# Kernel tuning notes

Hardware: AMD Instinct MI355X
Metric: run time of the kernel (lower is better)

## Reference

```python
import jax, jax.numpy as jnp
import numpy as np

OUT_F, IN_F = 4096, 4096
BLOCK = 64  # bitsandbytes NF4 block size

# NF4 code table (bitsandbytes): 16 quantile levels of a standard normal, scaled to [-1, 1]
NF4_CODE = jnp.array([
    -1.0, -0.6961928009986877, -0.5250730514526367, -0.39491748809814453,
    -0.28444138169288635, -0.18477343022823334, -0.09105003625154495, 0.0,
    0.07958029955625534, 0.16093020141124725, 0.24611230194568634, 0.33791524171829224,
    0.44070982933044434, 0.5626170039176941, 0.7229568362236023, 1.0,
], dtype=jnp.float32)


def dequantize_nf4(packed, absmax):
    # packed: [OUT_F*IN_F//2] int values in [0,256); two 4-bit indices per byte (high nibble first)
    hi = (packed >> 4) & 0xF
    lo = packed & 0xF
    idx = jnp.stack([hi, lo], axis=-1).reshape(-1)           # [OUT_F*IN_F]
    vals = NF4_CODE[idx]                                      # lookup
    vals = vals.reshape(-1, BLOCK) * absmax[:, None]          # per-block scale
    return vals.reshape(OUT_F, IN_F)


def setup_inputs() -> dict:
    key = jax.random.key(0)
    k1, k2, k3, k4 = jax.random.split(key, 4)
    x = jax.random.normal(k1, (4, 2048, IN_F), dtype=jnp.float32)
    packed_weight = jax.random.randint(k2, (OUT_F * IN_F // 2,), 0, 256, dtype=jnp.int32)
    absmax = jax.random.uniform(k3, (OUT_F * IN_F // BLOCK,), dtype=jnp.float32)
    bias = jax.random.normal(k4, (OUT_F,), dtype=jnp.float32)
    return {"x": x, "packed_weight": packed_weight, "absmax": absmax, "bias": bias}


def reference(x, packed_weight, absmax, bias):
    weight = dequantize_nf4(packed_weight, absmax)            # [OUT_F, IN_F]
    # F.linear: x @ W^T + b
    return jnp.einsum('bsi,oi->bso', x, weight) + bias
```

## Files before the change

kernel.cpp:

```cpp
#include <hip/hip_runtime.h>
#include <hip/hip_bf16.h>
#include <stdint.h>

#define IN_F   4096
#define OUT_F  4096
#define MROWS  8192

typedef __bf16 bf16x8 __attribute__((ext_vector_type(8)));
typedef float  f32x4  __attribute__((ext_vector_type(4)));
typedef unsigned short ushort8v __attribute__((ext_vector_type(8)));

__device__ __constant__ float NF4_TAB[16] = {
    -1.0f, -0.6961928009986877f, -0.5250730514526367f, -0.39491748809814453f,
    -0.28444138169288635f, -0.18477343022823334f, -0.09105003625154495f, 0.0f,
    0.07958029955625534f, 0.16093020141124725f, 0.24611230194568634f, 0.33791524171829224f,
    0.44070982933044434f, 0.5626170039176941f, 0.7229568362236023f, 1.0f,
};

__device__ __forceinline__ unsigned short f2bf_rne(float f) {
    unsigned u = __builtin_bit_cast(unsigned, f);
    return (unsigned short)((u + 0x7FFFu + ((u >> 16) & 1u)) >> 16);
}

__global__ void dequant_nf4_kernel(const int* __restrict__ packed,
                                   const float* __restrict__ absmax,
                                   unsigned short* __restrict__ wout,
                                   int ngroups) {
    int stride = gridDim.x * blockDim.x;
    for (int g = blockIdx.x * blockDim.x + threadIdx.x; g < ngroups; g += stride) {
        int4 pv = reinterpret_cast<const int4*>(packed)[g];
        float am = absmax[g >> 3];
        int p0 = pv.x, p1 = pv.y, p2 = pv.z, p3 = pv.w;
        ushort8v o;
        o[0] = f2bf_rne(NF4_TAB[(p0 >> 4) & 0xF] * am);
        o[1] = f2bf_rne(NF4_TAB[ p0       & 0xF] * am);
        o[2] = f2bf_rne(NF4_TAB[(p1 >> 4) & 0xF] * am);
        o[3] = f2bf_rne(NF4_TAB[ p1       & 0xF] * am);
        o[4] = f2bf_rne(NF4_TAB[(p2 >> 4) & 0xF] * am);
        o[5] = f2bf_rne(NF4_TAB[ p2       & 0xF] * am);
        o[6] = f2bf_rne(NF4_TAB[(p3 >> 4) & 0xF] * am);
        o[7] = f2bf_rne(NF4_TAB[ p3       & 0xF] * am);
        *reinterpret_cast<ushort8v*>(&wout[(size_t)g * 8]) = o;
    }
}

__global__ void cvt_f32_bf16_kernel(const float* __restrict__ in,
                                    unsigned short* __restrict__ out,
                                    int ngroups) {
    int stride = gridDim.x * blockDim.x;
    for (int g = blockIdx.x * blockDim.x + threadIdx.x; g < ngroups; g += stride) {
        float4 v = reinterpret_cast<const float4*>(in)[g];
        ushort4 o;
        o.x = f2bf_rne(v.x);
        o.y = f2bf_rne(v.y);
        o.z = f2bf_rne(v.z);
        o.w = f2bf_rne(v.w);
        reinterpret_cast<ushort4*>(out)[g] = o;
    }
}

#define GLOAD16(gp, lp)                                                        \
    __builtin_amdgcn_global_load_lds(                                          \
        (const __attribute__((address_space(1))) void*)(gp),                   \
        (__attribute__((address_space(3))) void*)(lp), 16, 0, 0)

__global__ __launch_bounds__(256) void gemm_bf16_kernel(
        const unsigned short* __restrict__ A,
        const unsigned short* __restrict__ B,
        const float* __restrict__ bias,
        float* __restrict__ C) {
    __shared__ __align__(16) unsigned short As[128 * 32];
    __shared__ __align__(16) unsigned short Bs[128 * 32];

    const int tid  = threadIdx.x;
    const int lane = tid & 63;
    const int wave = tid >> 6;
    const int wr = wave >> 1;
    const int wc = wave & 1;
    const int lr = lane & 15;
    const int lg = lane >> 4;

    const int bn = (blockIdx.x & 31) << 7;
    const int bm = (blockIdx.x >> 5) << 7;

    f32x4 acc[4][4] = {};

    const int c1 = tid, c2 = tid + 256;
    const int r1 = c1 >> 2, k1 = (c1 & 3) * 8;
    const int r2 = c2 >> 2, k2 = (c2 & 3) * 8;
    const unsigned short* Ag1 = A + (size_t)(bm + r1) * IN_F + k1;
    const unsigned short* Ag2 = A + (size_t)(bm + r2) * IN_F + k2;
    const unsigned short* Bg1 = B + (size_t)(bn + r1) * IN_F + k1;
    const unsigned short* Bg2 = B + (size_t)(bn + r2) * IN_F + k2;

    for (int k0 = 0; k0 < IN_F; k0 += 32) {
        GLOAD16(Ag1 + k0, &As[c1 * 8]);
        GLOAD16(Ag2 + k0, &As[c2 * 8]);
        GLOAD16(Bg1 + k0, &Bs[c1 * 8]);
        GLOAD16(Bg2 + k0, &Bs[c2 * 8]);
        __syncthreads();

        bf16x8 af[4], bfv[4];
#pragma unroll
        for (int mi = 0; mi < 4; ++mi)
            af[mi] = *reinterpret_cast<const bf16x8*>(
                &As[(wr * 64 + mi * 16 + lr) * 32 + lg * 8]);
#pragma unroll
        for (int ni = 0; ni < 4; ++ni)
            bfv[ni] = *reinterpret_cast<const bf16x8*>(
                &Bs[(wc * 64 + ni * 16 + lr) * 32 + lg * 8]);

#pragma unroll
        for (int mi = 0; mi < 4; ++mi)
#pragma unroll
            for (int ni = 0; ni < 4; ++ni)
                acc[mi][ni] = __builtin_amdgcn_mfma_f32_16x16x32_bf16(
                    af[mi], bfv[ni], acc[mi][ni], 0, 0, 0);

        __syncthreads();
    }

#pragma unroll
    for (int mi = 0; mi < 4; ++mi) {
        const int row0 = bm + wr * 64 + mi * 16 + lg * 4;
#pragma unroll
        for (int ni = 0; ni < 4; ++ni) {
            const int col = bn + wc * 64 + ni * 16 + lr;
            const float bs = bias[col];
            float* cp = C + (size_t)row0 * OUT_F + col;
#pragma unroll
            for (int j = 0; j < 4; ++j)
                cp[(size_t)j * OUT_F] = acc[mi][ni][j] + bs;
        }
    }
}

extern "C" void kernel_launch(void* const* d_in, const int* in_sizes, int n_in,
                              void* d_out, int out_size, void* d_ws, size_t ws_size,
                              hipStream_t stream) {
    const float* x      = (const float*)d_in[0];
    const int*   packed = (const int*)d_in[1];
    const float* absmax = (const float*)d_in[2];
    const float* bias   = (const float*)d_in[3];
    float* out = (float*)d_out;

    unsigned short* Wb = (unsigned short*)d_ws;
    unsigned short* Xb = Wb + (size_t)OUT_F * IN_F;

    const int npacked_groups = (OUT_F * IN_F / 2) / 4;
    const int ncvt_groups    = (MROWS * IN_F) / 4;

    dequant_nf4_kernel<<<2048, 256, 0, stream>>>(packed, absmax, Wb, npacked_groups);
    cvt_f32_bf16_kernel<<<2048, 256, 0, stream>>>(x, Xb, ncvt_groups);
    gemm_bf16_kernel<<<dim3(2048), dim3(256), 0, stream>>>(Xb, Wb, bias, out);
}
```

Baseline: 556.5 us.

## Merge prep kernels and replace GEMM with 256x256 double-buffered swizzled kernel

Combines weight dequantization and activation bf16 conversion into one launch that splits blocks between the two jobs, with the NF4 table copied into shared memory. The GEMM moves from 128x128 tiles with a single LDS buffer to 256x256 tiles on 512 threads, using a double-buffered 128KB LDS pipeline, XOR-swizzled layout, staged prefetch with explicit vmcnt/lgkmcnt waits, setprio around MFMA bursts, and a remapped block order for L2 locality. The aim is more data reuse per tile and overlap of global loads with MFMA work. In exchange it uses many more registers and all LDS, so occupancy drops to one block per CU, and the hand-written wait counts are fragile.

```diff
diff --git a/kernel.cpp b/kernel.cpp
--- a/kernel.cpp
+++ b/kernel.cpp
@@ -5,6 +5,7 @@
 #define IN_F   4096
 #define OUT_F  4096
 #define MROWS  8192
+#define NT     64
 
 typedef __bf16 bf16x8 __attribute__((ext_vector_type(8)));
 typedef float  f32x4  __attribute__((ext_vector_type(4)));
@@ -22,40 +23,45 @@
     return (unsigned short)((u + 0x7FFFu + ((u >> 16) & 1u)) >> 16);
 }
 
-__global__ void dequant_nf4_kernel(const int* __restrict__ packed,
-                                   const float* __restrict__ absmax,
-                                   unsigned short* __restrict__ wout,
-                                   int ngroups) {
-    int stride = gridDim.x * blockDim.x;
-    for (int g = blockIdx.x * blockDim.x + threadIdx.x; g < ngroups; g += stride) {
-        int4 pv = reinterpret_cast<const int4*>(packed)[g];
-        float am = absmax[g >> 3];
-        int p0 = pv.x, p1 = pv.y, p2 = pv.z, p3 = pv.w;
-        ushort8v o;
-        o[0] = f2bf_rne(NF4_TAB[(p0 >> 4) & 0xF] * am);
-        o[1] = f2bf_rne(NF4_TAB[ p0       & 0xF] * am);
-        o[2] = f2bf_rne(NF4_TAB[(p1 >> 4) & 0xF] * am);
-        o[3] = f2bf_rne(NF4_TAB[ p1       & 0xF] * am);
-        o[4] = f2bf_rne(NF4_TAB[(p2 >> 4) & 0xF] * am);
-        o[5] = f2bf_rne(NF4_TAB[ p2       & 0xF] * am);
-        o[6] = f2bf_rne(NF4_TAB[(p3 >> 4) & 0xF] * am);
-        o[7] = f2bf_rne(NF4_TAB[ p3       & 0xF] * am);
-        *reinterpret_cast<ushort8v*>(&wout[(size_t)g * 8]) = o;
-    }
-}
-
-__global__ void cvt_f32_bf16_kernel(const float* __restrict__ in,
-                                    unsigned short* __restrict__ out,
-                                    int ngroups) {
-    int stride = gridDim.x * blockDim.x;
-    for (int g = blockIdx.x * blockDim.x + threadIdx.x; g < ngroups; g += stride) {
-        float4 v = reinterpret_cast<const float4*>(in)[g];
-        ushort4 o;
-        o.x = f2bf_rne(v.x);
-        o.y = f2bf_rne(v.y);
-        o.z = f2bf_rne(v.z);
-        o.w = f2bf_rne(v.w);
-        reinterpret_cast<ushort4*>(out)[g] = o;
+__global__ __launch_bounds__(256) void prep_kernel(
+        const float* __restrict__ x, const int* __restrict__ packed,
+        const float* __restrict__ absmax,
+        unsigned short* __restrict__ Wb, unsigned short* __restrict__ Xb) {
+    __shared__ float tab[16];
+    if (threadIdx.x < 16) tab[threadIdx.x] = NF4_TAB[threadIdx.x];
+    __syncthreads();
+
+    const int bid = blockIdx.x;
+    if (bid < 512) {
+        const int ngroups = OUT_F * IN_F / 8;
+        const int stride = 512 * 256;
+        for (int g = bid * 256 + threadIdx.x; g < ngroups; g += stride) {
+            int4 pv = reinterpret_cast<const int4*>(packed)[g];
+            float am = absmax[g >> 3];
+            ushort8v o;
+            o[0] = f2bf_rne(tab[(pv.x >> 4) & 0xF] * am);
+            o[1] = f2bf_rne(tab[ pv.x       & 0xF] * am);
+            o[2] = f2bf_rne(tab[(pv.y >> 4) & 0xF] * am);
+            o[3] = f2bf_rne(tab[ pv.y       & 0xF] * am);
+            o[4] = f2bf_rne(tab[(pv.z >> 4) & 0xF] * am);
+            o[5] = f2bf_rne(tab[ pv.z       & 0xF] * am);
+            o[6] = f2bf_rne(tab[(pv.w >> 4) & 0xF] * am);
+            o[7] = f2bf_rne(tab[ pv.w       & 0xF] * am);
+            *reinterpret_cast<ushort8v*>(&Wb[(size_t)g * 8]) = o;
+        }
+    } else {
+        const int ngroups = MROWS * IN_F / 8;
+        const int stride = 1536 * 256;
+        for (int g = (bid - 512) * 256 + threadIdx.x; g < ngroups; g += stride) {
+            float4 v0 = reinterpret_cast<const float4*>(x)[2 * g];
+            float4 v1 = reinterpret_cast<const float4*>(x)[2 * g + 1];
+            ushort8v o;
+            o[0] = f2bf_rne(v0.x); o[1] = f2bf_rne(v0.y);
+            o[2] = f2bf_rne(v0.z); o[3] = f2bf_rne(v0.w);
+            o[4] = f2bf_rne(v1.x); o[5] = f2bf_rne(v1.y);
+            o[6] = f2bf_rne(v1.z); o[7] = f2bf_rne(v1.w);
+            *reinterpret_cast<ushort8v*>(&Xb[(size_t)g * 8]) = o;
+        }
     }
 }
 
@@ -64,73 +70,130 @@
         (const __attribute__((address_space(1))) void*)(gp),                   \
         (__attribute__((address_space(3))) void*)(lp), 16, 0, 0)
 
-__global__ __launch_bounds__(256) void gemm_bf16_kernel(
+#define BAR()   __builtin_amdgcn_s_barrier()
+#define LGKM0() do { asm volatile("s_waitcnt lgkmcnt(0)" ::: "memory");        \
+                     __builtin_amdgcn_sched_barrier(0); } while (0)
+#define VMW(n)  asm volatile("s_waitcnt vmcnt(" #n ")" ::: "memory")
+
+__global__ __launch_bounds__(512) void gemm256_kernel(
         const unsigned short* __restrict__ A,
         const unsigned short* __restrict__ B,
         const float* __restrict__ bias,
         float* __restrict__ C) {
-    __shared__ __align__(16) unsigned short As[128 * 32];
-    __shared__ __align__(16) unsigned short Bs[128 * 32];
+    __shared__ __align__(16) unsigned short lds[65536];
 
     const int tid  = threadIdx.x;
     const int lane = tid & 63;
     const int wave = tid >> 6;
-    const int wr = wave >> 1;
-    const int wc = wave & 1;
-    const int lr = lane & 15;
-    const int lg = lane >> 4;
-
-    const int bn = (blockIdx.x & 31) << 7;
-    const int bm = (blockIdx.x >> 5) << 7;
-
-    f32x4 acc[4][4] = {};
-
-    const int c1 = tid, c2 = tid + 256;
-    const int r1 = c1 >> 2, k1 = (c1 & 3) * 8;
-    const int r2 = c2 >> 2, k2 = (c2 & 3) * 8;
-    const unsigned short* Ag1 = A + (size_t)(bm + r1) * IN_F + k1;
-    const unsigned short* Ag2 = A + (size_t)(bm + r2) * IN_F + k2;
-    const unsigned short* Bg1 = B + (size_t)(bn + r1) * IN_F + k1;
-    const unsigned short* Bg2 = B + (size_t)(bn + r2) * IN_F + k2;
-
-    for (int k0 = 0; k0 < IN_F; k0 += 32) {
-        GLOAD16(Ag1 + k0, &As[c1 * 8]);
-        GLOAD16(Ag2 + k0, &As[c2 * 8]);
-        GLOAD16(Bg1 + k0, &Bs[c1 * 8]);
-        GLOAD16(Bg2 + k0, &Bs[c2 * 8]);
-        __syncthreads();
-
-        bf16x8 af[4], bfv[4];
-#pragma unroll
-        for (int mi = 0; mi < 4; ++mi)
-            af[mi] = *reinterpret_cast<const bf16x8*>(
-                &As[(wr * 64 + mi * 16 + lr) * 32 + lg * 8]);
-#pragma unroll
-        for (int ni = 0; ni < 4; ++ni)
-            bfv[ni] = *reinterpret_cast<const bf16x8*>(
-                &Bs[(wc * 64 + ni * 16 + lr) * 32 + lg * 8]);
-
-#pragma unroll
-        for (int mi = 0; mi < 4; ++mi)
-#pragma unroll
-            for (int ni = 0; ni < 4; ++ni)
-                acc[mi][ni] = __builtin_amdgcn_mfma_f32_16x16x32_bf16(
-                    af[mi], bfv[ni], acc[mi][ni], 0, 0, 0);
-
-        __syncthreads();
-    }
-
-#pragma unroll
-    for (int mi = 0; mi < 4; ++mi) {
-        const int row0 = bm + wr * 64 + mi * 16 + lg * 4;
+    const int wr   = wave >> 2;
+    const int wcn  = wave & 3;
+    const int lr   = lane & 15;
+    const int lg   = lane >> 4;
+
+    const int bid = blockIdx.x;
+    const int wg  = (bid & 7) * 64 + (bid >> 3);
+    const int bm  = (wg >> 4) << 8;
+    const int bn  = (wg & 15) << 8;
+
+    int srow[2], skel[2];
+#pragma unroll
+    for (int r = 0; r < 2; ++r) {
+        int c = tid + r * 512;
+        int L = c * 16;
+        int sw = L ^ (((L >> 7) & 7) << 4);
+        srow[r] = sw >> 6;
+        skel[r] = (sw & 63) >> 1;
+    }
+    const unsigned short* pA0 = A + (size_t)(bm + srow[0]) * IN_F + skel[0];
+    const unsigned short* pA1 = A + (size_t)(bm + srow[1]) * IN_F + skel[1];
+    const unsigned short* pB0 = B + (size_t)(bn + srow[0]) * IN_F + skel[0];
+    const unsigned short* pB1 = B + (size_t)(bn + srow[1]) * IN_F + skel[1];
+    const int d0 = tid * 8, d1 = tid * 8 + 4096;
+
+#define STAGE_A(t, kh) do {                                                    \
+        int _b = ((t) & 1) * 32768 + (kh) * 8192;                              \
+        int _k = (t) * 64 + (kh) * 32;                                         \
+        GLOAD16(pA0 + _k, &lds[_b + d0]);                                      \
+        GLOAD16(pA1 + _k, &lds[_b + d1]); } while (0)
+#define STAGE_B(t, kh) do {                                                    \
+        int _b = ((t) & 1) * 32768 + 16384 + (kh) * 8192;                      \
+        int _k = (t) * 64 + (kh) * 32;                                         \
+        GLOAD16(pB0 + _k, &lds[_b + d0]);                                      \
+        GLOAD16(pB1 + _k, &lds[_b + d1]); } while (0)
+
+    const int laneoff = ((lr * 64 + lg * 16) ^ (((lr >> 1) & 7) << 4)) >> 1;
+    const int arow = wr * 128;
+    const int brow = wcn * 64;
+
+    f32x4  acc[8][4] = {};
+    bf16x8 af[4], bfv[4];
+
+#define LOADB(b, kh) do {                                                      \
+        int _base = (b) * 32768 + 16384 + (kh) * 8192 + brow * 32 + laneoff;   \
+        bfv[0] = *reinterpret_cast<const bf16x8*>(&lds[_base]);                \
+        bfv[1] = *reinterpret_cast<const bf16x8*>(&lds[_base + 512]);          \
+        bfv[2] = *reinterpret_cast<const bf16x8*>(&lds[_base + 1024]);         \
+        bfv[3] = *reinterpret_cast<const bf16x8*>(&lds[_base + 1536]); } while (0)
+#define LOADA(b, kh, mq) do {                                                  \
+        int _base = (b) * 32768 + (kh) * 8192 + (arow + (mq) * 64) * 32 + laneoff; \
+        af[0] = *reinterpret_cast<const bf16x8*>(&lds[_base]);                 \
+        af[1] = *reinterpret_cast<const bf16x8*>(&lds[_base + 512]);           \
+        af[2] = *reinterpret_cast<const bf16x8*>(&lds[_base + 1024]);          \
+        af[3] = *reinterpret_cast<const bf16x8*>(&lds[_base + 1536]); } while (0)
+
+#define MFMA16(mq) do {                                                        \
+        __builtin_amdgcn_s_setprio(1);                                         \
+        _Pragma("unroll")                                                      \
+        for (int mi = 0; mi < 4; ++mi)                                         \
+            _Pragma("unroll")                                                  \
+            for (int ni = 0; ni < 4; ++ni)                                     \
+                acc[(mq) * 4 + mi][ni] = __builtin_amdgcn_mfma_f32_16x16x32_bf16( \
+                    af[mi], bfv[ni], acc[(mq) * 4 + mi][ni], 0, 0, 0);         \
+        __builtin_amdgcn_s_setprio(0); } while (0)
+
+    STAGE_B(0, 0); STAGE_A(0, 0); STAGE_B(0, 1); STAGE_A(0, 1);
+    STAGE_B(1, 0); STAGE_A(1, 0); STAGE_B(1, 1);
+    VMW(6);
+    BAR();
+
+#pragma unroll 2
+    for (int t = 0; t < NT; ++t) {
+        const int b = t & 1;
+        LOADB(b, 0); LOADA(b, 0, 0);
+        if (t + 1 < NT) STAGE_A(t + 1, 1);
+        BAR(); LGKM0();
+        MFMA16(0);
+        BAR();
+        LOADA(b, 0, 1);
+        if (t + 2 < NT) STAGE_B(t + 2, 0);
+        BAR(); LGKM0();
+        MFMA16(1);
+        BAR();
+        LOADB(b, 1); LOADA(b, 1, 0);
+        if (t + 2 < NT) STAGE_A(t + 2, 0);
+        BAR(); LGKM0();
+        MFMA16(0);
+        BAR();
+        LOADA(b, 1, 1);
+        if (t + 2 < NT) STAGE_B(t + 2, 1);
+        BAR(); LGKM0();
+        MFMA16(1);
+        if (t < NT - 2)       { VMW(6); }
+        else if (t == NT - 2) { VMW(0); }
+        BAR();
+    }
+
+#pragma unroll
+    for (int a = 0; a < 8; ++a) {
+        const int row0 = bm + wr * 128 + (a >> 2) * 64 + (a & 3) * 16 + lg * 4;
 #pragma unroll
         for (int ni = 0; ni < 4; ++ni) {
-            const int col = bn + wc * 64 + ni * 16 + lr;
+            const int col = bn + wcn * 64 + ni * 16 + lr;
             const float bs = bias[col];
             float* cp = C + (size_t)row0 * OUT_F + col;
 #pragma unroll
             for (int j = 0; j < 4; ++j)
-                cp[(size_t)j * OUT_F] = acc[mi][ni][j] + bs;
+                cp[(size_t)j * OUT_F] = acc[a][ni][j] + bs;
         }
     }
 }
@@ -147,10 +210,6 @@
     unsigned short* Wb = (unsigned short*)d_ws;
     unsigned short* Xb = Wb + (size_t)OUT_F * IN_F;
 
-    const int npacked_groups = (OUT_F * IN_F / 2) / 4;
-    const int ncvt_groups    = (MROWS * IN_F) / 4;
-
-    dequant_nf4_kernel<<<2048, 256, 0, stream>>>(packed, absmax, Wb, npacked_groups);
-    cvt_f32_bf16_kernel<<<2048, 256, 0, stream>>>(x, Xb, ncvt_groups);
-    gemm_bf16_kernel<<<dim3(2048), dim3(256), 0, stream>>>(Xb, Wb, bias, out);
-}
+    prep_kernel<<<2048, 256, 0, stream>>>(x, packed, absmax, Wb, Xb);
+    gemm256_kernel<<<512, 512, 0, stream>>>(Xb, Wb, bias, out);
+}
```

New measurement: 508.4 us. 1.09x faster.
